# Kernel tuning notes

Measured on AMD Instinct MI355X. Metric: run time of the kernel, lower is better.

The kernel has to match this reference:

```python
import jax, jax.numpy as jnp
import numpy as np

N_QUBITS = 4
N_LAYERS = 3
BATCH = 1048576  # 2**20; batched state vector [B, 2,2,2,2] complex64 = 128 MB


def setup_inputs() -> dict:
    key = jax.random.key(0)
    k1, k2 = jax.random.split(key)
    x = jax.random.normal(k1, (BATCH, N_QUBITS), dtype=jnp.float32)
    q_weights = jax.random.normal(k2, (N_LAYERS, N_QUBITS, 3), dtype=jnp.float32) * 0.1
    return {"x": x, "q_weights": q_weights}


def _ry_mat(theta):
    # RY(t) = [[cos t/2, -sin t/2], [sin t/2, cos t/2]]; theta: [] or [B]
    c = jnp.cos(theta * 0.5).astype(jnp.complex64)
    s = jnp.sin(theta * 0.5).astype(jnp.complex64)
    return jnp.stack([jnp.stack([c, -s], -1), jnp.stack([s, c], -1)], -2)


def _rz_mat(theta):
    # RZ(t) = diag(e^{-it/2}, e^{it/2})
    e = jnp.exp(-0.5j * theta.astype(jnp.complex64))
    z = jnp.zeros_like(e)
    return jnp.stack([jnp.stack([e, z], -1), jnp.stack([z, jnp.conj(e)], -1)], -2)


def _apply_1q(state, U, wire):
    # state: [B,2,2,2,2]; U: [2,2] (shared) or [B,2,2] (per-sample)
    ax = wire + 1
    state = jnp.moveaxis(state, ax, -1)
    if U.ndim == 3:
        state = jnp.einsum('b...o,bno->b...n', state, U)
    else:
        state = jnp.einsum('b...o,no->b...n', state, U)
    return jnp.moveaxis(state, -1, ax)


def _cnot(state, c, t):
    # flip target bit on the control=1 slice
    ca, ta = c + 1, t + 1
    s0 = jnp.take(state, 0, axis=ca)
    s1 = jnp.take(state, 1, axis=ca)
    ta2 = ta if ta < ca else ta - 1
    s1 = jnp.flip(s1, axis=ta2)
    return jnp.stack([s0, s1], axis=ca)


def _circuit(x, q_weights):
    B = x.shape[0]
    xn = jnp.tanh(x) * jnp.pi  # [B, 4]
    # |0000>
    state = jnp.zeros((B,) + (2,) * N_QUBITS, dtype=jnp.complex64)
    state = state.at[:, 0, 0, 0, 0].set(1.0 + 0.0j)
    # angle encoding: RY(2x_i) then RZ(x_i), per-sample batched 2x2 gates
    for i in range(N_QUBITS):
        state = _apply_1q(state, _ry_mat(2.0 * xn[:, i]), i)
        state = _apply_1q(state, _rz_mat(xn[:, i]), i)
    # variational layers: Rot(phi,theta,omega) = RZ(omega) @ RY(theta) @ RZ(phi)
    for l in range(N_LAYERS):
        for i in range(N_QUBITS):
            phi, theta, omega = q_weights[l, i, 0], q_weights[l, i, 1], q_weights[l, i, 2]
            U = _rz_mat(omega) @ _ry_mat(theta) @ _rz_mat(phi)
            state = _apply_1q(state, U, i)
        for i in range(N_QUBITS):
            state = _cnot(state, i, (i + 1) % N_QUBITS)
    # <Z_i> = p(bit_i=0) - p(bit_i=1)
    probs = jnp.abs(state) ** 2  # [B,2,2,2,2] real
    evs = []
    for i in range(N_QUBITS):
        axes = tuple(a for a in range(1, N_QUBITS + 1) if a != i + 1)
        marg = jnp.sum(probs, axis=axes)  # [B, 2]
        evs.append(marg[:, 0] - marg[:, 1])
    return jnp.stack(evs, axis=-1).astype(jnp.float32)  # [B, 4]


def reference(x, q_weights):
    return _circuit(x, q_weights)
```

## Files before the change

### kernel.cpp

```cpp
#include <hip/hip_runtime.h>

#define PI_F 3.14159265358979323846f

__device__ __forceinline__ float2 cmadd2(float2 u, float2 a, float2 w, float2 b) {
    float re = fmaf(u.x, a.x, fmaf(-u.y, a.y, fmaf(w.x, b.x, -(w.y * b.y))));
    float im = fmaf(u.x, a.y, fmaf(u.y, a.x, fmaf(w.x, b.y, w.y * b.x)));
    return make_float2(re, im);
}
__device__ __forceinline__ float2 cmul(float2 a, float2 b) {
    return make_float2(fmaf(a.x, b.x, -(a.y * b.y)), fmaf(a.x, b.y, a.y * b.x));
}

template <int BP>
__device__ __forceinline__ void apply_gate(float2 st[16], float2 u00, float2 u01,
                                           float2 u10, float2 u11) {
#pragma unroll
    for (int i = 0; i < 8; i++) {
        const int lo = ((i >> BP) << (BP + 1)) | (i & ((1 << BP) - 1));
        const int hi = lo | (1 << BP);
        float2 a = st[lo], b = st[hi];
        st[lo] = cmadd2(u00, a, u01, b);
        st[hi] = cmadd2(u10, a, u11, b);
    }
}

template <int CB, int TB>
__device__ __forceinline__ void cnot(float2 st[16]) {
#pragma unroll
    for (int i = 0; i < 16; i++) {
        if ((i & (1 << CB)) && !(i & (1 << TB))) {
            float2 t = st[i];
            st[i] = st[i | (1 << TB)];
            st[i | (1 << TB)] = t;
        }
    }
}

__global__ __launch_bounds__(256) void qlayer_kernel(const float* __restrict__ x,
                                                     const float* __restrict__ qw,
                                                     float* __restrict__ out, int B) {
    __shared__ float4 Ug[12][2];
    const int tid = threadIdx.x;
    if (tid < 12) {
        const float phi = qw[tid * 3 + 0];
        const float th  = qw[tid * 3 + 1];
        const float om  = qw[tid * 3 + 2];
        float s, c;   __sincosf(0.5f * th, &s, &c);
        float sa, ca; __sincosf(0.5f * (phi + om), &sa, &ca);
        float sb, cb; __sincosf(0.5f * (phi - om), &sb, &cb);
        Ug[tid][0] = make_float4(c * ca, -c * sa, -s * cb, -s * sb);
        Ug[tid][1] = make_float4(s * cb, -s * sb, c * ca, c * sa);
    }
    __syncthreads();

    const int b = blockIdx.x * 256 + tid;
    if (b >= B) return;

    const float4 xv = reinterpret_cast<const float4*>(x)[b];
    const float xs[4] = {xv.x, xv.y, xv.z, xv.w};

    float2 v[4][2];
#pragma unroll
    for (int q = 0; q < 4; q++) {
        const float xq = xs[q];
        const float ax = fabsf(xq);
        const float e  = __builtin_amdgcn_exp2f(ax * -2.8853900817779268f);
        const float r  = __builtin_amdgcn_rcpf(1.0f + e);
        const float t  = copysignf((1.0f - e) * r, xq);
        const float sh = __builtin_amdgcn_sinf(t * 0.25f);
        const float ch = __builtin_amdgcn_cosf(t * 0.25f);
        const float s  = 2.0f * sh * ch;
        const float c  = fmaf(-2.0f * sh, sh, 1.0f);
        v[q][0] = make_float2(c * ch, -(c * sh));
        v[q][1] = make_float2(s * ch, s * sh);
    }

#pragma unroll
    for (int q = 0; q < 4; q++) {
        const float4 A = Ug[q][0], Bq = Ug[q][1];
        const float2 u00 = make_float2(A.x, A.y),  u01 = make_float2(A.z, A.w);
        const float2 u10 = make_float2(Bq.x, Bq.y), u11 = make_float2(Bq.z, Bq.w);
        const float2 a = v[q][0], bb = v[q][1];
        v[q][0] = cmadd2(u00, a, u01, bb);
        v[q][1] = cmadd2(u10, a, u11, bb);
    }

    float2 t01[4], t23[4];
#pragma unroll
    for (int i = 0; i < 4; i++) {
        t01[i] = cmul(v[0][(i >> 1) & 1], v[1][i & 1]);
        t23[i] = cmul(v[2][(i >> 1) & 1], v[3][i & 1]);
    }
    float2 st[16];
#pragma unroll
    for (int i = 0; i < 16; i++) st[i] = cmul(t01[i >> 2], t23[i & 3]);

    cnot<3, 2>(st); cnot<2, 1>(st); cnot<1, 0>(st); cnot<0, 3>(st);

#pragma unroll
    for (int l = 1; l < 3; l++) {
#pragma unroll
        for (int q = 0; q < 4; q++) {
            const int g = l * 4 + q;
            const float4 A = Ug[g][0], Bq = Ug[g][1];
            const float2 u00 = make_float2(A.x, A.y),  u01 = make_float2(A.z, A.w);
            const float2 u10 = make_float2(Bq.x, Bq.y), u11 = make_float2(Bq.z, Bq.w);
            switch (q) {
                case 0: apply_gate<3>(st, u00, u01, u10, u11); break;
                case 1: apply_gate<2>(st, u00, u01, u10, u11); break;
                case 2: apply_gate<1>(st, u00, u01, u10, u11); break;
                case 3: apply_gate<0>(st, u00, u01, u10, u11); break;
            }
        }
        cnot<3, 2>(st); cnot<2, 1>(st); cnot<1, 0>(st); cnot<0, 3>(st);
    }

    float p[16];
#pragma unroll
    for (int i = 0; i < 16; i++) p[i] = fmaf(st[i].x, st[i].x, st[i].y * st[i].y);

    float pr[8];
#pragma unroll
    for (int j = 0; j < 8; j++) pr[j] = p[2 * j] + p[2 * j + 1];

    const float s3 = (pr[4] + pr[5]) + (pr[6] + pr[7]);
    const float s2 = (pr[2] + pr[3]) + (pr[6] + pr[7]);
    const float s1 = (pr[1] + pr[3]) + (pr[5] + pr[7]);
    const float s0 = ((p[1] + p[3]) + (p[5] + p[7])) +
                     ((p[9] + p[11]) + (p[13] + p[15]));

    float4 ev;
    ev.x = fmaf(-2.0f, s3, 1.0f);
    ev.y = fmaf(-2.0f, s2, 1.0f);
    ev.z = fmaf(-2.0f, s1, 1.0f);
    ev.w = fmaf(-2.0f, s0, 1.0f);
    reinterpret_cast<float4*>(out)[b] = ev;
}

extern "C" void kernel_launch(void* const* d_in, const int* in_sizes, int n_in,
                              void* d_out, int out_size, void* d_ws, size_t ws_size,
                              hipStream_t stream) {
    const float* x  = (const float*)d_in[0];
    const float* qw = (const float*)d_in[1];
    float* out = (float*)d_out;
    const int B = in_sizes[0] / 4;
    const int blocks = (B + 255) / 256;
    qlayer_kernel<<<blocks, 256, 0, stream>>>(x, qw, out, B);
}
```

Baseline: 96.65 us.

## Process two samples per thread with packed float2 math

Each thread now simulates two batch samples, keeping them side by side in float2 lanes (structure-of-arrays re/im pairs). The point is to let the compiler emit packed FP32 instructions (v_pk_fma_f32/v_pk_mul_f32) on CDNA, which would roughly halve the instruction count per sample, and to spread the shared-memory gate loads over two samples. The grid is halved to match. In exchange, register pressure per thread roughly doubles, which can lower occupancy, and the tail needs a guarded second store.

```diff
diff --git a/kernel.cpp b/kernel.cpp
--- a/kernel.cpp
+++ b/kernel.cpp
@@ -1,39 +1,71 @@
 #include <hip/hip_runtime.h>
 
-#define PI_F 3.14159265358979323846f
+struct P { float2 re, im; };
 
-__device__ __forceinline__ float2 cmadd2(float2 u, float2 a, float2 w, float2 b) {
-    float re = fmaf(u.x, a.x, fmaf(-u.y, a.y, fmaf(w.x, b.x, -(w.y * b.y))));
-    float im = fmaf(u.x, a.y, fmaf(u.y, a.x, fmaf(w.x, b.y, w.y * b.x)));
-    return make_float2(re, im);
+__device__ __forceinline__ float2 f2(float x, float y) { return make_float2(x, y); }
+__device__ __forceinline__ float2 splat(float s) { return make_float2(s, s); }
+__device__ __forceinline__ float2 add2(float2 a, float2 b) { return f2(a.x + b.x, a.y + b.y); }
+__device__ __forceinline__ float2 mul2(float2 a, float2 b) { return f2(a.x * b.x, a.y * b.y); }
+__device__ __forceinline__ float2 neg2(float2 a) { return f2(-a.x, -a.y); }
+__device__ __forceinline__ float2 fma2(float2 a, float2 b, float2 c) {
+    return f2(fmaf(a.x, b.x, c.x), fmaf(a.y, b.y, c.y));
 }
-__device__ __forceinline__ float2 cmul(float2 a, float2 b) {
-    return make_float2(fmaf(a.x, b.x, -(a.y * b.y)), fmaf(a.x, b.y, a.y * b.x));
+
+__device__ __forceinline__ P cmadd2p(float2 u, float2 w, const P& a, const P& b) {
+    P r;
+    r.re = fma2(splat(u.x), a.re,
+           fma2(splat(-u.y), a.im,
+           fma2(splat(w.x), b.re, mul2(splat(-w.y), b.im))));
+    r.im = fma2(splat(u.x), a.im,
+           fma2(splat(u.y), a.re,
+           fma2(splat(w.x), b.im, mul2(splat(w.y), b.re))));
+    return r;
+}
+
+__device__ __forceinline__ P cmulp(const P& a, const P& b) {
+    P r;
+    r.re = fma2(a.re, b.re, mul2(neg2(a.im), b.im));
+    r.im = fma2(a.re, b.im, mul2(a.im, b.re));
+    return r;
 }
 
 template <int BP>
-__device__ __forceinline__ void apply_gate(float2 st[16], float2 u00, float2 u01,
-                                           float2 u10, float2 u11) {
+__device__ __forceinline__ void apply_gate(P st[16], float4 A4, float4 B4) {
+    const float2 u00 = f2(A4.x, A4.y), u01 = f2(A4.z, A4.w);
+    const float2 u10 = f2(B4.x, B4.y), u11 = f2(B4.z, B4.w);
 #pragma unroll
     for (int i = 0; i < 8; i++) {
         const int lo = ((i >> BP) << (BP + 1)) | (i & ((1 << BP) - 1));
         const int hi = lo | (1 << BP);
-        float2 a = st[lo], b = st[hi];
-        st[lo] = cmadd2(u00, a, u01, b);
-        st[hi] = cmadd2(u10, a, u11, b);
+        const P a = st[lo], b = st[hi];
+        st[lo] = cmadd2p(u00, u01, a, b);
+        st[hi] = cmadd2p(u10, u11, a, b);
     }
 }
 
 template <int CB, int TB>
-__device__ __forceinline__ void cnot(float2 st[16]) {
+__device__ __forceinline__ void cnot(P st[16]) {
 #pragma unroll
     for (int i = 0; i < 16; i++) {
         if ((i & (1 << CB)) && !(i & (1 << TB))) {
-            float2 t = st[i];
+            P t = st[i];
             st[i] = st[i | (1 << TB)];
             st[i | (1 << TB)] = t;
         }
     }
+}
+
+struct Enc { float r0, i0, r1, i1; };
+__device__ __forceinline__ Enc encode(float xq) {
+    const float ax = fabsf(xq);
+    const float e  = __builtin_amdgcn_exp2f(ax * -2.8853900817779268f);
+    const float r  = __builtin_amdgcn_rcpf(1.0f + e);
+    const float t  = copysignf((1.0f - e) * r, xq);
+    const float sh = __builtin_amdgcn_sinf(t * 0.25f);
+    const float ch = __builtin_amdgcn_cosf(t * 0.25f);
+    const float s  = 2.0f * sh * ch;
+    const float c  = fmaf(-2.0f * sh, sh, 1.0f);
+    return {c * ch, -(c * sh), s * ch, s * sh};
 }
 
 __global__ __launch_bounds__(256) void qlayer_kernel(const float* __restrict__ x,
@@ -53,88 +85,74 @@
     }
     __syncthreads();
 
-    const int b = blockIdx.x * 256 + tid;
-    if (b >= B) return;
+    const int bA = blockIdx.x * 512 + tid;
+    if (bA >= B) return;
+    const int bB0 = bA + 256;
+    const bool hasB = bB0 < B;
+    const int bB = hasB ? bB0 : bA;
 
-    const float4 xv = reinterpret_cast<const float4*>(x)[b];
-    const float xs[4] = {xv.x, xv.y, xv.z, xv.w};
+    const float4 xA = reinterpret_cast<const float4*>(x)[bA];
+    const float4 xB = reinterpret_cast<const float4*>(x)[bB];
+    const float xsA[4] = {xA.x, xA.y, xA.z, xA.w};
+    const float xsB[4] = {xB.x, xB.y, xB.z, xB.w};
 
-    float2 v[4][2];
+    P v[4][2];
 #pragma unroll
     for (int q = 0; q < 4; q++) {
-        const float xq = xs[q];
-        const float ax = fabsf(xq);
-        const float e  = __builtin_amdgcn_exp2f(ax * -2.8853900817779268f);
-        const float r  = __builtin_amdgcn_rcpf(1.0f + e);
-        const float t  = copysignf((1.0f - e) * r, xq);
-        const float sh = __builtin_amdgcn_sinf(t * 0.25f);
-        const float ch = __builtin_amdgcn_cosf(t * 0.25f);
-        const float s  = 2.0f * sh * ch;
-        const float c  = fmaf(-2.0f * sh, sh, 1.0f);
-        v[q][0] = make_float2(c * ch, -(c * sh));
-        v[q][1] = make_float2(s * ch, s * sh);
+        const Enc eA = encode(xsA[q]);
+        const Enc eB = encode(xsB[q]);
+        P a; a.re = f2(eA.r0, eB.r0); a.im = f2(eA.i0, eB.i0);
+        P b; b.re = f2(eA.r1, eB.r1); b.im = f2(eA.i1, eB.i1);
+        const float4 A4 = Ug[q][0], B4 = Ug[q][1];
+        v[q][0] = cmadd2p(f2(A4.x, A4.y), f2(A4.z, A4.w), a, b);
+        v[q][1] = cmadd2p(f2(B4.x, B4.y), f2(B4.z, B4.w), a, b);
     }
 
-#pragma unroll
-    for (int q = 0; q < 4; q++) {
-        const float4 A = Ug[q][0], Bq = Ug[q][1];
-        const float2 u00 = make_float2(A.x, A.y),  u01 = make_float2(A.z, A.w);
-        const float2 u10 = make_float2(Bq.x, Bq.y), u11 = make_float2(Bq.z, Bq.w);
-        const float2 a = v[q][0], bb = v[q][1];
-        v[q][0] = cmadd2(u00, a, u01, bb);
-        v[q][1] = cmadd2(u10, a, u11, bb);
-    }
-
-    float2 t01[4], t23[4];
+    P t01[4], t23[4];
 #pragma unroll
     for (int i = 0; i < 4; i++) {
-        t01[i] = cmul(v[0][(i >> 1) & 1], v[1][i & 1]);
-        t23[i] = cmul(v[2][(i >> 1) & 1], v[3][i & 1]);
+        t01[i] = cmulp(v[0][(i >> 1) & 1], v[1][i & 1]);
+        t23[i] = cmulp(v[2][(i >> 1) & 1], v[3][i & 1]);
     }
-    float2 st[16];
+    P st[16];
 #pragma unroll
-    for (int i = 0; i < 16; i++) st[i] = cmul(t01[i >> 2], t23[i & 3]);
+    for (int i = 0; i < 16; i++) st[i] = cmulp(t01[i >> 2], t23[i & 3]);
 
     cnot<3, 2>(st); cnot<2, 1>(st); cnot<1, 0>(st); cnot<0, 3>(st);
 
+    apply_gate<3>(st, Ug[4][0], Ug[4][1]);
+    apply_gate<2>(st, Ug[5][0], Ug[5][1]);
+    apply_gate<1>(st, Ug[6][0], Ug[6][1]);
+    apply_gate<0>(st, Ug[7][0], Ug[7][1]);
+    cnot<3, 2>(st); cnot<2, 1>(st); cnot<1, 0>(st); cnot<0, 3>(st);
+    apply_gate<3>(st, Ug[8][0], Ug[8][1]);
+    apply_gate<2>(st, Ug[9][0], Ug[9][1]);
+    apply_gate<1>(st, Ug[10][0], Ug[10][1]);
+    apply_gate<0>(st, Ug[11][0], Ug[11][1]);
+    cnot<3, 2>(st); cnot<2, 1>(st); cnot<1, 0>(st); cnot<0, 3>(st);
+
+    float2 p[16];
 #pragma unroll
-    for (int l = 1; l < 3; l++) {
+    for (int i = 0; i < 16; i++) p[i] = fma2(st[i].re, st[i].re, mul2(st[i].im, st[i].im));
+
+    float2 pr[8];
 #pragma unroll
-        for (int q = 0; q < 4; q++) {
-            const int g = l * 4 + q;
-            const float4 A = Ug[g][0], Bq = Ug[g][1];
-            const float2 u00 = make_float2(A.x, A.y),  u01 = make_float2(A.z, A.w);
-            const float2 u10 = make_float2(Bq.x, Bq.y), u11 = make_float2(Bq.z, Bq.w);
-            switch (q) {
-                case 0: apply_gate<3>(st, u00, u01, u10, u11); break;
-                case 1: apply_gate<2>(st, u00, u01, u10, u11); break;
-                case 2: apply_gate<1>(st, u00, u01, u10, u11); break;
-                case 3: apply_gate<0>(st, u00, u01, u10, u11); break;
-            }
-        }
-        cnot<3, 2>(st); cnot<2, 1>(st); cnot<1, 0>(st); cnot<0, 3>(st);
-    }
+    for (int j = 0; j < 8; j++) pr[j] = add2(p[2 * j], p[2 * j + 1]);
 
-    float p[16];
-#pragma unroll
-    for (int i = 0; i < 16; i++) p[i] = fmaf(st[i].x, st[i].x, st[i].y * st[i].y);
+    const float2 s3 = add2(add2(pr[4], pr[5]), add2(pr[6], pr[7]));
+    const float2 s2 = add2(add2(pr[2], pr[3]), add2(pr[6], pr[7]));
+    const float2 s1 = add2(add2(pr[1], pr[3]), add2(pr[5], pr[7]));
+    const float2 s0 = add2(add2(add2(p[1], p[3]), add2(p[5], p[7])),
+                           add2(add2(p[9], p[11]), add2(p[13], p[15])));
 
-    float pr[8];
-#pragma unroll
-    for (int j = 0; j < 8; j++) pr[j] = p[2 * j] + p[2 * j + 1];
+    float4 evA, evB;
+    evA.x = fmaf(-2.0f, s3.x, 1.0f); evB.x = fmaf(-2.0f, s3.y, 1.0f);
+    evA.y = fmaf(-2.0f, s2.x, 1.0f); evB.y = fmaf(-2.0f, s2.y, 1.0f);
+    evA.z = fmaf(-2.0f, s1.x, 1.0f); evB.z = fmaf(-2.0f, s1.y, 1.0f);
+    evA.w = fmaf(-2.0f, s0.x, 1.0f); evB.w = fmaf(-2.0f, s0.y, 1.0f);
 
-    const float s3 = (pr[4] + pr[5]) + (pr[6] + pr[7]);
-    const float s2 = (pr[2] + pr[3]) + (pr[6] + pr[7]);
-    const float s1 = (pr[1] + pr[3]) + (pr[5] + pr[7]);
-    const float s0 = ((p[1] + p[3]) + (p[5] + p[7])) +
-                     ((p[9] + p[11]) + (p[13] + p[15]));
-
-    float4 ev;
-    ev.x = fmaf(-2.0f, s3, 1.0f);
-    ev.y = fmaf(-2.0f, s2, 1.0f);
-    ev.z = fmaf(-2.0f, s1, 1.0f);
-    ev.w = fmaf(-2.0f, s0, 1.0f);
-    reinterpret_cast<float4*>(out)[b] = ev;
+    reinterpret_cast<float4*>(out)[bA] = evA;
+    if (hasB) reinterpret_cast<float4*>(out)[bB0] = evB;
 }
 
 extern "C" void kernel_launch(void* const* d_in, const int* in_sizes, int n_in,
@@ -144,6 +162,6 @@
     const float* qw = (const float*)d_in[1];
     float* out = (float*)d_out;
     const int B = in_sizes[0] / 4;
-    const int blocks = (B + 255) / 256;
+    const int blocks = (B + 511) / 512;
     qlayer_kernel<<<blocks, 256, 0, stream>>>(x, qw, out, B);
 }
```

After: 95.46 us. About the same (-1.2%).
